# Performance work log

Measured on AMD Instinct MI355X. Metric: run time of the kernel, lower is better.

Reference implementation:

```python
import jax, jax.numpy as jnp
import numpy as np

N = 4194304          # pixels (e.g. 2048x2048 render)
MOTION = 8
H = 8
OUT = 3
N_LAYERS = 3
Z_SCALE = 10.0
INV_SQRT_2PI = 1.0 / np.sqrt(2.0 * np.pi)

# activation set chosen from Fun.funs: sin, gaus, tanh, id
FUNS = [
    jnp.sin,
    lambda t: INV_SQRT_2PI * jnp.exp(-0.5 * t * t),  # 'gaus'
    jnp.tanh,
    lambda t: t,                                      # 'id'
]


def _make_masks(rng):
    # mirror __init__: per layer, permute H cells and split into len(Funs) sorted groups
    masks = []
    for _ in range(N_LAYERS):
        perm = rng.permutation(H)
        masks.append([np.sort(a) for a in np.array_split(perm, len(FUNS))])
    return jnp.asarray(np.array(masks), dtype=jnp.int64)  # [L, F, H/F]


def setup_inputs() -> dict:
    key = jax.random.key(0)
    ks = jax.random.split(key, 10)
    rng = np.random.default_rng(0)
    return {
        "x": jax.random.normal(ks[0], (N, 1), jnp.float32),
        "y": jax.random.normal(ks[1], (N, 1), jnp.float32),
        "r": jax.random.uniform(ks[2], (N, 1), jnp.float32),
        "z": jax.random.normal(ks[3], (N, MOTION), jnp.float32),
        "W0": jax.random.normal(ks[4], (H, MOTION + 3), jnp.float32) * 0.3,
        "b0": jax.random.normal(ks[5], (H,), jnp.float32) * 0.1,
        "Wm": jax.random.normal(ks[6], (H, H), jnp.float32) * 0.3,
        "bm": jax.random.normal(ks[7], (H,), jnp.float32) * 0.1,
        "Wo": jax.random.normal(ks[8], (OUT, H), jnp.float32) * 0.3,
        "bo": jax.random.normal(ks[9], (OUT,), jnp.float32) * 0.1,
        "masks": _make_masks(rng),
    }


def reference(x, y, r, z, W0, b0, Wm, bm, Wo, bo, masks):
    inp = jnp.concatenate([z / Z_SCALE, x, y, r], axis=1)  # [N, MOTION+3]
    out = inp @ W0.T + b0                                  # [N, H]
    for l in range(N_LAYERS):
        # NOTE: original repeats the same Linear module -> shared Wm/bm across layers
        pre = out @ Wm.T + bm
        new_out = jnp.zeros_like(out)
        for f, fn in enumerate(FUNS):
            m = masks[l, f]                                # disjoint column group
            new_out = new_out.at[:, m].set(fn(pre[:, m]))
        out = (new_out + out) * 0.5
    return jax.nn.sigmoid(out @ Wo.T + bo)                 # [N, OUT]
```

## Files before the change

kernel.cpp:

```cpp
#include <hip/hip_runtime.h>


__global__ void cppn_prep(const float* __restrict__ W0,
                          const float* __restrict__ b0,
                          const float* __restrict__ Wm,
                          const float* __restrict__ bm,
                          const float* __restrict__ Wo,
                          const float* __restrict__ bo,
                          const int* __restrict__ masks,
                          float* __restrict__ wf,
                          int* __restrict__ wi) {
    int t = threadIdx.x;
    if (t < 88) {
        int k = t % 11;
        wf[t] = W0[t] * (k < 8 ? 0.1f : 1.0f);
    } else if (t < 96) {
        wf[t] = b0[t - 88];
    } else if (t < 288) {
        int j = t - 96;
        int l = j >> 6;
        float s = (l == 0) ? 1.0f : (l == 1 ? 0.5f : 0.25f);
        wf[96 + j] = Wm[j & 63] * s;
    } else if (t < 296) {
        wf[t] = bm[t - 288];
    } else if (t < 320) {
        wf[t] = Wo[t - 296] * 0.125f;
    } else if (t < 323) {
        wf[t] = bo[t - 320];
    } else if (t < 323 + 24) {
        int j = t - 323;
        bool is64 = true;
        for (int q = 1; q < 24; q += 2) is64 = is64 && (masks[q] == 0);
        int c = is64 ? masks[2 * j] : masks[j];
        int l = j >> 3;
        int f = (j & 7) >> 1;
        wi[384 + l * 8 + c] = f;
    }
}

#define PX 2

__global__ __launch_bounds__(256) void cppn_main(
    const float* __restrict__ xb,
    const float* __restrict__ yb,
    const float* __restrict__ rb,
    const float4* __restrict__ zb,
    const float* __restrict__ wf,
    const int* __restrict__ fid,
    float* __restrict__ out,
    int n) {
    int base = blockIdx.x * (256 * PX) + threadIdx.x;
    int idx[PX];
    bool ok[PX];
#pragma unroll
    for (int px = 0; px < PX; ++px) {
        idx[px] = base + px * 256;
        ok[px] = idx[px] < n;
    }

    float in[PX][11];
#pragma unroll
    for (int px = 0; px < PX; ++px) {
        int i = ok[px] ? idx[px] : 0;
        float4 z0 = zb[2 * i];
        float4 z1 = zb[2 * i + 1];
        in[px][0] = z0.x; in[px][1] = z0.y; in[px][2] = z0.z; in[px][3] = z0.w;
        in[px][4] = z1.x; in[px][5] = z1.y; in[px][6] = z1.z; in[px][7] = z1.w;
        in[px][8]  = xb[i];
        in[px][9]  = yb[i];
        in[px][10] = rb[i];
    }

    float u[PX][8];
#pragma unroll
    for (int h = 0; h < 8; ++h) {
#pragma unroll
        for (int px = 0; px < PX; ++px) {
            float acc = wf[88 + h];
#pragma unroll
            for (int k = 0; k < 11; ++k)
                acc = fmaf(wf[h * 11 + k], in[px][k], acc);
            u[px][h] = acc;
        }
    }

#pragma unroll
    for (int l = 0; l < 3; ++l) {
        const float* W = wf + 96 + 64 * l;
        const float scale = (l == 0) ? 1.0f : (l == 1 ? 2.0f : 4.0f);
        float p[PX][8];
#pragma unroll
        for (int h = 0; h < 8; ++h) {
#pragma unroll
            for (int px = 0; px < PX; ++px) {
                float acc = wf[288 + h];
#pragma unroll
                for (int k = 0; k < 8; ++k)
                    acc = fmaf(W[h * 8 + k], u[px][k], acc);
                p[px][h] = acc;
            }
        }
#pragma unroll
        for (int h = 0; h < 8; ++h) {
            int f = __builtin_amdgcn_readfirstlane(fid[l * 8 + h]);
            float v[PX];
            if (f == 0) {
#pragma unroll
                for (int px = 0; px < PX; ++px) v[px] = __sinf(p[px][h]);
            } else if (f == 1) {
#pragma unroll
                for (int px = 0; px < PX; ++px) {
                    float t = p[px][h];
                    v[px] = 0.3989422804014327f * __expf(-0.5f * t * t);
                }
            } else if (f == 2) {
#pragma unroll
                for (int px = 0; px < PX; ++px) {
                    float e = __expf(2.0f * p[px][h]);
                    v[px] = fmaf(-2.0f, __builtin_amdgcn_rcpf(e + 1.0f), 1.0f);
                }
            } else {
#pragma unroll
                for (int px = 0; px < PX; ++px) v[px] = p[px][h];
            }
#pragma unroll
            for (int px = 0; px < PX; ++px)
                u[px][h] = fmaf(scale, v[px], u[px][h]);
        }
    }

#pragma unroll
    for (int j = 0; j < 3; ++j) {
#pragma unroll
        for (int px = 0; px < PX; ++px) {
            float acc = wf[320 + j];
#pragma unroll
            for (int k = 0; k < 8; ++k)
                acc = fmaf(wf[296 + j * 8 + k], u[px][k], acc);
            float e = __expf(-acc);
            float v = __builtin_amdgcn_rcpf(1.0f + e);
            if (ok[px]) out[3 * idx[px] + j] = v;
        }
    }
}

extern "C" void kernel_launch(void* const* d_in, const int* in_sizes, int n_in,
                              void* d_out, int out_size, void* d_ws, size_t ws_size,
                              hipStream_t stream) {
    const float* xb = (const float*)d_in[0];
    const float* yb = (const float*)d_in[1];
    const float* rb = (const float*)d_in[2];
    const float* zb = (const float*)d_in[3];
    const float* W0 = (const float*)d_in[4];
    const float* b0 = (const float*)d_in[5];
    const float* Wm = (const float*)d_in[6];
    const float* bm = (const float*)d_in[7];
    const float* Wo = (const float*)d_in[8];
    const float* bo = (const float*)d_in[9];
    const int* masks = (const int*)d_in[10];

    float* wf = (float*)d_ws;
    int*   wi = (int*)d_ws;

    int n = in_sizes[0];

    cppn_prep<<<1, 512, 0, stream>>>(W0, b0, Wm, bm, Wo, bo, masks, wf, wi);
    int per_block = 256 * PX;
    cppn_main<<<(n + per_block - 1) / per_block, 256, 0, stream>>>(
        xb, yb, rb, (const float4*)zb, wf, wi + 384,
        (float*)d_out, n);
}
```

Measured before the change: 258.8 us.

## Process adjacent pixel pairs per thread with float2 vectorized loads and stores

Each thread now handles two consecutive pixels instead of two pixels strided by 256. This lets x/y/r be read as float2, z as four contiguous float4, and the 6 outputs written as three float2 stores. Math is expressed on float2 pairs, which could let the compiler emit packed FMA (v_pk_fma_f32). The cost is less coalesced z access per wavefront (each thread reads 64 contiguous bytes) and a tail path for odd n.

Result: no change. 263.6 us (+1.9%).

```diff
diff --git a/kernel.cpp b/kernel.cpp
--- a/kernel.cpp
+++ b/kernel.cpp
@@ -38,109 +38,121 @@
     }
 }
 
-#define PX 2
+static __device__ __forceinline__ float2 fma2(float s, float2 a, float2 c) {
+    return make_float2(fmaf(s, a.x, c.x), fmaf(s, a.y, c.y));
+}
 
 __global__ __launch_bounds__(256) void cppn_main(
     const float* __restrict__ xb,
     const float* __restrict__ yb,
     const float* __restrict__ rb,
-    const float4* __restrict__ zb,
+    const float4* __restrict__ z4,
     const float* __restrict__ wf,
     const int* __restrict__ fid,
     float* __restrict__ out,
     int n) {
-    int base = blockIdx.x * (256 * PX) + threadIdx.x;
-    int idx[PX];
-    bool ok[PX];
-#pragma unroll
-    for (int px = 0; px < PX; ++px) {
-        idx[px] = base + px * 256;
-        ok[px] = idx[px] < n;
+    int t = blockIdx.x * 256 + threadIdx.x;
+    int p0 = 2 * t;
+    if (p0 >= n) return;
+    bool ok1 = (p0 + 1) < n;
+
+    float4 za = z4[4 * t];
+    float4 zc = z4[4 * t + 1];
+    float4 zbv, zdv;
+    float2 xv, yv, rv;
+    if (ok1) {
+        zbv = z4[4 * t + 2];
+        zdv = z4[4 * t + 3];
+        xv = ((const float2*)xb)[t];
+        yv = ((const float2*)yb)[t];
+        rv = ((const float2*)rb)[t];
+    } else {
+        zbv = za; zdv = zc;
+        xv = make_float2(xb[p0], xb[p0]);
+        yv = make_float2(yb[p0], yb[p0]);
+        rv = make_float2(rb[p0], rb[p0]);
     }
 
-    float in[PX][11];
-#pragma unroll
-    for (int px = 0; px < PX; ++px) {
-        int i = ok[px] ? idx[px] : 0;
-        float4 z0 = zb[2 * i];
-        float4 z1 = zb[2 * i + 1];
-        in[px][0] = z0.x; in[px][1] = z0.y; in[px][2] = z0.z; in[px][3] = z0.w;
-        in[px][4] = z1.x; in[px][5] = z1.y; in[px][6] = z1.z; in[px][7] = z1.w;
-        in[px][8]  = xb[i];
-        in[px][9]  = yb[i];
-        in[px][10] = rb[i];
-    }
+    float2 in2[11];
+    in2[0] = make_float2(za.x, zbv.x);
+    in2[1] = make_float2(za.y, zbv.y);
+    in2[2] = make_float2(za.z, zbv.z);
+    in2[3] = make_float2(za.w, zbv.w);
+    in2[4] = make_float2(zc.x, zdv.x);
+    in2[5] = make_float2(zc.y, zdv.y);
+    in2[6] = make_float2(zc.z, zdv.z);
+    in2[7] = make_float2(zc.w, zdv.w);
+    in2[8]  = xv;
+    in2[9]  = yv;
+    in2[10] = rv;
 
-    float u[PX][8];
+    float2 u[8];
 #pragma unroll
     for (int h = 0; h < 8; ++h) {
+        float2 acc = make_float2(wf[88 + h], wf[88 + h]);
 #pragma unroll
-        for (int px = 0; px < PX; ++px) {
-            float acc = wf[88 + h];
-#pragma unroll
-            for (int k = 0; k < 11; ++k)
-                acc = fmaf(wf[h * 11 + k], in[px][k], acc);
-            u[px][h] = acc;
-        }
+        for (int k = 0; k < 11; ++k)
+            acc = fma2(wf[h * 11 + k], in2[k], acc);
+        u[h] = acc;
     }
 
 #pragma unroll
     for (int l = 0; l < 3; ++l) {
         const float* W = wf + 96 + 64 * l;
         const float scale = (l == 0) ? 1.0f : (l == 1 ? 2.0f : 4.0f);
-        float p[PX][8];
+        float2 p[8];
 #pragma unroll
         for (int h = 0; h < 8; ++h) {
+            float2 acc = make_float2(wf[288 + h], wf[288 + h]);
 #pragma unroll
-            for (int px = 0; px < PX; ++px) {
-                float acc = wf[288 + h];
-#pragma unroll
-                for (int k = 0; k < 8; ++k)
-                    acc = fmaf(W[h * 8 + k], u[px][k], acc);
-                p[px][h] = acc;
-            }
+            for (int k = 0; k < 8; ++k)
+                acc = fma2(W[h * 8 + k], u[k], acc);
+            p[h] = acc;
         }
 #pragma unroll
         for (int h = 0; h < 8; ++h) {
             int f = __builtin_amdgcn_readfirstlane(fid[l * 8 + h]);
-            float v[PX];
+            float2 v;
             if (f == 0) {
-#pragma unroll
-                for (int px = 0; px < PX; ++px) v[px] = __sinf(p[px][h]);
+                v = make_float2(__sinf(p[h].x), __sinf(p[h].y));
             } else if (f == 1) {
-#pragma unroll
-                for (int px = 0; px < PX; ++px) {
-                    float t = p[px][h];
-                    v[px] = 0.3989422804014327f * __expf(-0.5f * t * t);
-                }
+                v = make_float2(
+                    0.3989422804014327f * __expf(-0.5f * p[h].x * p[h].x),
+                    0.3989422804014327f * __expf(-0.5f * p[h].y * p[h].y));
             } else if (f == 2) {
-#pragma unroll
-                for (int px = 0; px < PX; ++px) {
-                    float e = __expf(2.0f * p[px][h]);
-                    v[px] = fmaf(-2.0f, __builtin_amdgcn_rcpf(e + 1.0f), 1.0f);
-                }
+                float ea = __expf(2.0f * p[h].x);
+                float eb = __expf(2.0f * p[h].y);
+                v = make_float2(
+                    fmaf(-2.0f, __builtin_amdgcn_rcpf(ea + 1.0f), 1.0f),
+                    fmaf(-2.0f, __builtin_amdgcn_rcpf(eb + 1.0f), 1.0f));
             } else {
-#pragma unroll
-                for (int px = 0; px < PX; ++px) v[px] = p[px][h];
+                v = p[h];
             }
-#pragma unroll
-            for (int px = 0; px < PX; ++px)
-                u[px][h] = fmaf(scale, v[px], u[px][h]);
+            u[h] = fma2(scale, v, u[h]);
         }
     }
 
+    float2 o[3];
 #pragma unroll
     for (int j = 0; j < 3; ++j) {
+        float2 acc = make_float2(wf[320 + j], wf[320 + j]);
 #pragma unroll
-        for (int px = 0; px < PX; ++px) {
-            float acc = wf[320 + j];
-#pragma unroll
-            for (int k = 0; k < 8; ++k)
-                acc = fmaf(wf[296 + j * 8 + k], u[px][k], acc);
-            float e = __expf(-acc);
-            float v = __builtin_amdgcn_rcpf(1.0f + e);
-            if (ok[px]) out[3 * idx[px] + j] = v;
-        }
+        for (int k = 0; k < 8; ++k)
+            acc = fma2(wf[296 + j * 8 + k], u[k], acc);
+        o[j] = make_float2(
+            __builtin_amdgcn_rcpf(1.0f + __expf(-acc.x)),
+            __builtin_amdgcn_rcpf(1.0f + __expf(-acc.y)));
+    }
+
+    if (ok1) {
+        float2* o2 = (float2*)out;
+        o2[3 * t]     = make_float2(o[0].x, o[1].x);
+        o2[3 * t + 1] = make_float2(o[2].x, o[0].y);
+        o2[3 * t + 2] = make_float2(o[1].y, o[2].y);
+    } else {
+        out[3 * p0]     = o[0].x;
+        out[3 * p0 + 1] = o[1].x;
+        out[3 * p0 + 2] = o[2].x;
     }
 }
 
@@ -165,7 +177,7 @@
     int n = in_sizes[0];
 
     cppn_prep<<<1, 512, 0, stream>>>(W0, b0, Wm, bm, Wo, bo, masks, wf, wi);
-    int per_block = 256 * PX;
+    int per_block = 512;
     cppn_main<<<(n + per_block - 1) / per_block, 256, 0, stream>>>(
         xb, yb, rb, (const float4*)zb, wf, wi + 384,
         (float*)d_out, n);
```
